# Kernel tuning notes

Hardware: AMD Instinct MI355X
Metric: run time of the kernel (lower is better)

The kernel has to match this reference:

```python
import jax, jax.numpy as jnp
import numpy as np

B = 8192          # batch rows
F0 = 2048         # base input features
E = 512           # embed rows added per recursion level
L = 3             # chain depth
OUT = 2048        # MAIN output dim
NNZ_E = 8192      # nnz per embed sparse weight (~16/row)
NNZ_M = 16384     # nnz of MAIN sparse weight (~8/row)


def _spmm_t(rows, cols, vals, x, n_rows):
    """Compute (W_sparse @ x.T).T = x @ W.T for COO W of shape [n_rows, x.shape[1]].
    out[b, r] = sum_{k: rows[k]==r} vals[k] * x[b, cols[k]]
    """
    contrib = x[:, cols] * vals                     # [B, nnz]
    return jax.ops.segment_sum(contrib.T, rows, num_segments=n_rows).T  # [B, n_rows]


def setup_inputs() -> dict:
    key = jax.random.key(0)
    ks = jax.random.split(key, 12)
    widths = [F0, F0 + E, F0 + 2 * E]               # input width at each recursion level
    inp = {"x": jax.random.normal(ks[0], (B, F0), dtype=jnp.float32)}
    for i, w in enumerate(widths):
        inp[f"emb_rows{i}"] = jax.random.randint(ks[1 + 3 * i], (NNZ_E,), 0, E, dtype=jnp.int32)
        inp[f"emb_cols{i}"] = jax.random.randint(ks[2 + 3 * i], (NNZ_E,), 0, w, dtype=jnp.int32)
        inp[f"emb_vals{i}"] = jax.random.normal(ks[3 + 3 * i], (NNZ_E,), dtype=jnp.float32)
    inp["main_rows"] = jax.random.randint(ks[10], (NNZ_M,), 0, OUT, dtype=jnp.int32)
    inp["main_cols"] = jax.random.randint(ks[11], (NNZ_M,), 0, F0 + 3 * E, dtype=jnp.int32)
    inp["main_vals"] = jax.random.normal(jax.random.fold_in(key, 99), (NNZ_M,), dtype=jnp.float32)
    return inp


def reference(x, emb_rows0, emb_cols0, emb_vals0,
              emb_rows1, emb_cols1, emb_vals1,
              emb_rows2, emb_cols2, emb_vals2,
              main_rows, main_cols, main_vals):
    # Recursive chain unrolled oldest-first: each level sparse-mms its embed
    # weight against the running input and concatenates the result.
    h = x
    for rows, cols, vals in ((emb_rows0, emb_cols0, emb_vals0),
                             (emb_rows1, emb_cols1, emb_vals1),
                             (emb_rows2, emb_cols2, emb_vals2)):
        e = _spmm_t(rows, cols, vals, h, E)         # [B, E]
        h = jnp.concatenate([h, e], axis=1)
    # is_last: pass concatenated features through the MAIN sparse linear
    return _spmm_t(main_rows, main_cols, main_vals, h, OUT)  # [B, OUT]
```

## Files before the change

kernel.cpp:

```cpp
#include <hip/hip_runtime.h>
#include <stdint.h>

#define F0    2048
#define EROWS 512
#define NOUT  2048
#define MROWS 8192

typedef __attribute__((ext_vector_type(8))) short bf16x8;
typedef __attribute__((ext_vector_type(4))) float f32x4;
typedef __attribute__((ext_vector_type(8))) unsigned short u16x8;

typedef const __attribute__((address_space(1))) unsigned char ga_t;
typedef __attribute__((address_space(3))) unsigned char lds_t;

__device__ __forceinline__ void async_load16(const void* g, void* l) {
  __builtin_amdgcn_global_load_lds((ga_t*)g, (lds_t*)l, 16, 0, 0);
}

__device__ __forceinline__ unsigned short f2bf(float f) {
  unsigned int u = __builtin_bit_cast(unsigned int, f);
  u += 0x7fffu + ((u >> 16) & 1u);
  return (unsigned short)(u >> 16);
}

__global__ __launch_bounds__(256) void csr_cast_kernel(
    const int* __restrict__ r0, const int* __restrict__ c0, const float* __restrict__ v0, int n0,
    const int* __restrict__ r1, const int* __restrict__ c1, const float* __restrict__ v1, int n1,
    const int* __restrict__ r2, const int* __restrict__ c2, const float* __restrict__ v2, int n2,
    const int* __restrict__ rm, const int* __restrict__ cm, const float* __restrict__ vm, int nm,
    int* __restrict__ rp_all, int* __restrict__ cc_all, float* __restrict__ cv_all,
    const float* __restrict__ x, unsigned short* __restrict__ Ab)
{
  const int b = blockIdx.x;
  const int tid = threadIdx.x;

  if (b >= 4) {
    const int cb = b - 4;
    const float4* xp = (const float4*)x;
    u16x8* ap = (u16x8*)Ab;
#pragma unroll
    for (int it = 0; it < 4; ++it) {
      int i = cb * 1024 + it * 256 + tid;
      float4 a = xp[2 * i], c = xp[2 * i + 1];
      u16x8 o;
      o[0] = f2bf(a.x); o[1] = f2bf(a.y); o[2] = f2bf(a.z); o[3] = f2bf(a.w);
      o[4] = f2bf(c.x); o[5] = f2bf(c.y); o[6] = f2bf(c.z); o[7] = f2bf(c.w);
      ap[i] = o;
    }
    return;
  }

  const int* rows; const int* cols; const float* vals; int nnz, nrows;
  if      (b == 0) { rows = r0; cols = c0; vals = v0; nnz = n0; nrows = EROWS; }
  else if (b == 1) { rows = r1; cols = c1; vals = v1; nnz = n1; nrows = EROWS; }
  else if (b == 2) { rows = r2; cols = c2; vals = v2; nnz = n2; nrows = EROWS; }
  else             { rows = rm; cols = cm; vals = vm; nnz = nm; nrows = NOUT; }
  int* rp  = rp_all + b * 4096;
  int* cc  = cc_all + b * 8192;
  float* cv = cv_all + b * 8192;

  __shared__ int hist[NOUT + 1];
  __shared__ int tsum[256];

  for (int i = tid; i < nrows; i += 256) hist[i] = 0;
  __syncthreads();

  int k0 = 0;
  for (; k0 + 2048 <= nnz; k0 += 2048) {
    const int kk = k0 + tid * 8;
    int4 ra = *(const int4*)(rows + kk);
    int4 rb = *(const int4*)(rows + kk + 4);
    atomicAdd(&hist[ra.x], 1); atomicAdd(&hist[ra.y], 1);
    atomicAdd(&hist[ra.z], 1); atomicAdd(&hist[ra.w], 1);
    atomicAdd(&hist[rb.x], 1); atomicAdd(&hist[rb.y], 1);
    atomicAdd(&hist[rb.z], 1); atomicAdd(&hist[rb.w], 1);
  }
  for (int k = k0 + tid; k < nnz; k += 256) atomicAdd(&hist[rows[k]], 1);
  __syncthreads();

  const int per = nrows >> 8;
  const int base = tid * per;
  int sum = 0;
  for (int i = 0; i < per; ++i) sum += hist[base + i];
  tsum[tid] = sum;
  __syncthreads();
  for (int off = 1; off < 256; off <<= 1) {
    int add = (tid >= off) ? tsum[tid - off] : 0;
    __syncthreads();
    tsum[tid] += add;
    __syncthreads();
  }
  int run = (tid == 0) ? 0 : tsum[tid - 1];
  for (int i = 0; i < per; ++i) { int h = hist[base + i]; hist[base + i] = run; run += h; }
  __syncthreads();

  for (int i = tid; i < nrows; i += 256) rp[i] = hist[i];
  if (tid == 0) rp[nrows] = nnz;
  __syncthreads();

  k0 = 0;
  for (; k0 + 2048 <= nnz; k0 += 2048) {
    const int kk = k0 + tid * 8;
    int4   ra = *(const int4*)(rows + kk);
    int4   rb = *(const int4*)(rows + kk + 4);
    int4   ca = *(const int4*)(cols + kk);
    int4   cb2 = *(const int4*)(cols + kk + 4);
    float4 va = *(const float4*)(vals + kk);
    float4 vb = *(const float4*)(vals + kk + 4);
    int p;
    p = atomicAdd(&hist[ra.x], 1); cc[p] = ca.x;  cv[p] = va.x;
    p = atomicAdd(&hist[ra.y], 1); cc[p] = ca.y;  cv[p] = va.y;
    p = atomicAdd(&hist[ra.z], 1); cc[p] = ca.z;  cv[p] = va.z;
    p = atomicAdd(&hist[ra.w], 1); cc[p] = ca.w;  cv[p] = va.w;
    p = atomicAdd(&hist[rb.x], 1); cc[p] = cb2.x; cv[p] = vb.x;
    p = atomicAdd(&hist[rb.y], 1); cc[p] = cb2.y; cv[p] = vb.y;
    p = atomicAdd(&hist[rb.z], 1); cc[p] = cb2.z; cv[p] = vb.z;
    p = atomicAdd(&hist[rb.w], 1); cc[p] = cb2.w; cv[p] = vb.w;
  }
  for (int k = k0 + tid; k < nnz; k += 256) {
    int p = atomicAdd(&hist[rows[k]], 1);
    cc[p] = cols[k]; cv[p] = vals[k];
  }
}

template <bool BF16OUT>
__global__ __launch_bounds__(256) void expand_csr_kernel(
    const int* __restrict__ rp, const int* __restrict__ cc,
    const float* __restrict__ cv, const float* __restrict__ Dsrc,
    void* __restrict__ out)
{
  const int r = blockIdx.x;
  const int tid = threadIdx.x;
  __shared__ float acc[F0];
  __shared__ int   icol[128];
  __shared__ float ival[128];
  __shared__ int   icnt;

  float4* a4 = (float4*)acc;
  a4[tid * 2]     = (float4){0.f, 0.f, 0.f, 0.f};
  a4[tid * 2 + 1] = (float4){0.f, 0.f, 0.f, 0.f};
  if (tid == 0) icnt = 0;
  __syncthreads();

  const int s = rp[r], e = rp[r + 1];
  for (int i = s + tid; i < e; i += 256) {
    int c = cc[i]; float v = cv[i];
    if (c < F0) atomicAdd(&acc[c], v);
    else { int p = atomicAdd(&icnt, 1); if (p < 128) { icol[p] = c - F0; ival[p] = v; } }
  }
  __syncthreads();
  int n = icnt; if (n > 128) n = 128;

  float4 q0 = a4[tid * 2], q1 = a4[tid * 2 + 1];
  for (int j = 0; j < n; ++j) {
    const float4* src = (const float4*)(Dsrc + (size_t)icol[j] * F0) + tid * 2;
    float v = ival[j];
    float4 s0 = src[0], s1 = src[1];
    q0.x += v * s0.x; q0.y += v * s0.y; q0.z += v * s0.z; q0.w += v * s0.w;
    q1.x += v * s1.x; q1.y += v * s1.y; q1.z += v * s1.z; q1.w += v * s1.w;
  }

  if (BF16OUT) {
    u16x8 o;
    o[0] = f2bf(q0.x); o[1] = f2bf(q0.y); o[2] = f2bf(q0.z); o[3] = f2bf(q0.w);
    o[4] = f2bf(q1.x); o[5] = f2bf(q1.y); o[6] = f2bf(q1.z); o[7] = f2bf(q1.w);
    ((u16x8*)out)[(size_t)r * 256 + tid] = o;
  } else {
    float4* dst = (float4*)out + (size_t)r * 512 + tid * 2;
    dst[0] = q0; dst[1] = q1;
  }
}

__global__ __launch_bounds__(512, 2) void gemm256_kernel(
    const unsigned short* __restrict__ A, const unsigned short* __restrict__ B,
    float* __restrict__ C)
{
  constexpr int K  = F0;
  constexpr int N  = NOUT;
  constexpr int NT = K / 64;

  extern __shared__ __align__(16) unsigned short lds[];
  unsigned short* sA = lds;
  unsigned short* sB = lds + 32768;

  const int tid  = threadIdx.x;
  const int lane = tid & 63;
  const int w    = tid >> 6;
  const int wr   = w >> 2;
  const int wc   = w & 3;
  const int mm   = lane & 15;
  const int g    = lane >> 4;
  const int sx   = mm & 7;
  const int bm   = blockIdx.y;
  const int bn   = blockIdx.x;

  const unsigned short* Ag = A + (size_t)bm * 256 * K;
  const unsigned short* Bg = B + (size_t)bn * 256 * K;

  const int    r0    = tid >> 3;
  const int    c0    = (tid & 7) ^ (r0 & 7);
  const size_t goff0 = (size_t)r0 * K + c0 * 8;
  const size_t goff1 = goff0 + (size_t)64 * K;
  const int    loff0 = tid * 8;
  const int    loff1 = 4096 + tid * 8;

#define STG(Gb, Sb, buf, h, t) do {                                           \
    async_load16((Gb) + goff0 + (size_t)(h) * 128 * K + (t) * 64,             \
                 (Sb) + (buf) * 16384 + (h) * 8192 + loff0);                  \
    async_load16((Gb) + goff1 + (size_t)(h) * 128 * K + (t) * 64,             \
                 (Sb) + (buf) * 16384 + (h) * 8192 + loff1);                  \
  } while (0)

  const unsigned short* paB = sA + (wr * 128 + mm) * 64;
  const unsigned short* pbB = sB + (wc * 64  + mm) * 64;
  const int s0 = ((0 * 4 + g) ^ sx) * 8;
  const int s1 = ((1 * 4 + g) ^ sx) * 8;

  bf16x8 af[4][2];
  bf16x8 bf0[2][2];
  bf16x8 bf1[2][2];

#define LDA(buf, qm) do {                                                     \
    const unsigned short* p_ = paB + (buf) * 16384 + (qm) * 4096;             \
    _Pragma("unroll") for (int tm = 0; tm < 4; ++tm) {                        \
      af[tm][0] = *(const bf16x8*)(p_ + tm * 1024 + s0);                      \
      af[tm][1] = *(const bf16x8*)(p_ + tm * 1024 + s1);                      \
    } } while (0)

#define LDB(dst, buf, qn) do {                                                \
    const unsigned short* p_ = pbB + (buf) * 16384 + (qn) * 2048;             \
    _Pragma("unroll") for (int tn = 0; tn < 2; ++tn) {                        \
      dst[tn][0] = *(const bf16x8*)(p_ + tn * 1024 + s0);                     \
      dst[tn][1] = *(const bf16x8*)(p_ + tn * 1024 + s1);                     \
    } } while (0)

#define PH_MFMA(qm, qn, bfX) do {                                             \
    __builtin_amdgcn_s_setprio(1);                                            \
    _Pragma("unroll") for (int tm = 0; tm < 4; ++tm)                          \
    _Pragma("unroll") for (int tn = 0; tn < 2; ++tn) {                        \
      acc[(qm)*4+tm][(qn)*2+tn] = __builtin_amdgcn_mfma_f32_16x16x32_bf16(    \
          af[tm][0], bfX[tn][0], acc[(qm)*4+tm][(qn)*2+tn], 0, 0, 0);         \
      acc[(qm)*4+tm][(qn)*2+tn] = __builtin_amdgcn_mfma_f32_16x16x32_bf16(    \
          af[tm][1], bfX[tn][1], acc[(qm)*4+tm][(qn)*2+tn], 0, 0, 0);         \
    }                                                                         \
    __builtin_amdgcn_s_setprio(0);                                            \
  } while (0)

#define BAR        __builtin_amdgcn_s_barrier()
#define LGKM0      asm volatile("s_waitcnt lgkmcnt(0)" ::: "memory")
#define WAIT_VM(n) asm volatile("s_waitcnt vmcnt(" #n ")" ::: "memory")

  f32x4 acc[8][4];
#pragma unroll
  for (int i = 0; i < 8; ++i)
#pragma unroll
    for (int j = 0; j < 4; ++j) acc[i][j] = (f32x4)0.f;

  STG(Ag, sA, 0, 0, 0); STG(Ag, sA, 0, 1, 0);
  STG(Bg, sB, 0, 0, 0); STG(Bg, sB, 0, 1, 0);
  STG(Bg, sB, 1, 0, 1); STG(Bg, sB, 1, 1, 1);
  STG(Ag, sA, 1, 0, 1);
  WAIT_VM(6);
  BAR;

#pragma unroll 2
  for (int t = 0; t < NT; ++t) {
    const int buf  = t & 1;
    const int nbuf = buf ^ 1;

    LDA(buf, 0); LDB(bf0, buf, 0);
    if (t + 1 < NT) STG(Ag, sA, nbuf, 1, t + 1);
    BAR; LGKM0;
    PH_MFMA(0, 0, bf0);
    BAR;

    LDB(bf1, buf, 1);
    BAR; LGKM0;
    PH_MFMA(0, 1, bf1);
    BAR;

    LDA(buf, 1);
    if (t + 2 < NT) STG(Bg, sB, buf, 0, t + 2);
    BAR; LGKM0;
    PH_MFMA(1, 1, bf1);
    BAR;

    if (t + 2 < NT) { STG(Bg, sB, buf, 1, t + 2);
                      STG(Ag, sA, buf, 0, t + 2); }
    BAR;
    PH_MFMA(1, 0, bf0);
    if      (t + 2 < NT) { WAIT_VM(6); }
    else if (t + 1 < NT) { WAIT_VM(0); }
    BAR;
  }

  const int rowb = bm * 256 + wr * 128 + g * 4;
  const int colb = bn * 256 + wc * 64 + mm;
#pragma unroll
  for (int im = 0; im < 8; ++im) {
#pragma unroll
    for (int in2 = 0; in2 < 4; ++in2) {
      const int row = rowb + im * 16;
      const int col = colb + in2 * 16;
#pragma unroll
      for (int r = 0; r < 4; ++r)
        C[(size_t)(row + r) * N + col] = acc[im][in2][r];
    }
  }

#undef STG
#undef LDA
#undef LDB
#undef PH_MFMA
#undef BAR
#undef LGKM0
#undef WAIT_VM
}

extern "C" void kernel_launch(void* const* d_in, const int* in_sizes, int n_in,
                              void* d_out, int out_size, void* d_ws, size_t ws_size,
                              hipStream_t stream)
{
  const float* x   = (const float*)d_in[0];
  const int*   er0 = (const int*)d_in[1];
  const int*   ec0 = (const int*)d_in[2];
  const float* ev0 = (const float*)d_in[3];
  const int*   er1 = (const int*)d_in[4];
  const int*   ec1 = (const int*)d_in[5];
  const float* ev1 = (const float*)d_in[6];
  const int*   er2 = (const int*)d_in[7];
  const int*   ec2 = (const int*)d_in[8];
  const float* ev2 = (const float*)d_in[9];
  const int*   mr  = (const int*)d_in[10];
  const int*   mc  = (const int*)d_in[11];
  const float* mv  = (const float*)d_in[12];
  const int nnz_e0 = in_sizes[1];
  const int nnz_e1 = in_sizes[4];
  const int nnz_e2 = in_sizes[7];
  const int nnz_m  = in_sizes[10];

  int*   rp_all = (int*)d_ws;
  int*   cc_all = rp_all + 4 * 4096;
  float* cv_all = (float*)(cc_all + 48 * 1024);
  float* D      = (float*)(cv_all + 48 * 1024);
  unsigned short* Mb = (unsigned short*)(D + (size_t)3 * EROWS * F0);
  unsigned short* Ab = Mb + (size_t)NOUT * F0;

  hipLaunchKernelGGL(csr_cast_kernel, dim3(4 + 2048), dim3(256), 0, stream,
                     er0, ec0, ev0, nnz_e0,
                     er1, ec1, ev1, nnz_e1,
                     er2, ec2, ev2, nnz_e2,
                     mr,  mc,  mv,  nnz_m,
                     rp_all, cc_all, cv_all, x, Ab);

  hipLaunchKernelGGL((expand_csr_kernel<false>), dim3(EROWS), dim3(256), 0, stream,
                     rp_all + 0 * 4096, cc_all + 0 * 8192, cv_all + 0 * 8192,
                     D, (void*)D);
  hipLaunchKernelGGL((expand_csr_kernel<false>), dim3(EROWS), dim3(256), 0, stream,
                     rp_all + 1 * 4096, cc_all + 1 * 8192, cv_all + 1 * 8192,
                     D, (void*)(D + (size_t)EROWS * F0));
  hipLaunchKernelGGL((expand_csr_kernel<false>), dim3(EROWS), dim3(256), 0, stream,
                     rp_all + 2 * 4096, cc_all + 2 * 8192, cv_all + 2 * 8192,
                     D, (void*)(D + (size_t)2 * EROWS * F0));
  hipLaunchKernelGGL((expand_csr_kernel<true>), dim3(NOUT), dim3(256), 0, stream,
                     rp_all + 3 * 4096, cc_all + 3 * 8192, cv_all + 3 * 8192,
                     D, (void*)Mb);

  hipFuncSetAttribute(reinterpret_cast<const void*>(gemm256_kernel),
                      hipFuncAttributeMaxDynamicSharedMemorySize, 131072);
  hipLaunchKernelGGL(gemm256_kernel, dim3(NOUT / 256, MROWS / 256), dim3(512),
                     131072, stream, Ab, Mb, (float*)d_out);
}
```

Measured before the change: 240.3 us.

## Spread x cast across expand kernels and software-pipeline GEMM LDS fragment loads

```diff
diff --git a/kernel.cpp b/kernel.cpp
--- a/kernel.cpp
+++ b/kernel.cpp
@@ -28,27 +28,10 @@
     const int* __restrict__ r1, const int* __restrict__ c1, const float* __restrict__ v1, int n1,
     const int* __restrict__ r2, const int* __restrict__ c2, const float* __restrict__ v2, int n2,
     const int* __restrict__ rm, const int* __restrict__ cm, const float* __restrict__ vm, int nm,
-    int* __restrict__ rp_all, int* __restrict__ cc_all, float* __restrict__ cv_all,
-    const float* __restrict__ x, unsigned short* __restrict__ Ab)
+    int* __restrict__ rp_all, int* __restrict__ cc_all, float* __restrict__ cv_all)
 {
   const int b = blockIdx.x;
   const int tid = threadIdx.x;
-
-  if (b >= 4) {
-    const int cb = b - 4;
-    const float4* xp = (const float4*)x;
-    u16x8* ap = (u16x8*)Ab;
-#pragma unroll
-    for (int it = 0; it < 4; ++it) {
-      int i = cb * 1024 + it * 256 + tid;
-      float4 a = xp[2 * i], c = xp[2 * i + 1];
-      u16x8 o;
-      o[0] = f2bf(a.x); o[1] = f2bf(a.y); o[2] = f2bf(a.z); o[3] = f2bf(a.w);
-      o[4] = f2bf(c.x); o[5] = f2bf(c.y); o[6] = f2bf(c.z); o[7] = f2bf(c.w);
-      ap[i] = o;
-    }
-    return;
-  }
 
   const int* rows; const int* cols; const float* vals; int nnz, nrows;
   if      (b == 0) { rows = r0; cols = c0; vals = v0; nnz = n0; nrows = EROWS; }
@@ -127,10 +110,29 @@
 __global__ __launch_bounds__(256) void expand_csr_kernel(
     const int* __restrict__ rp, const int* __restrict__ cc,
     const float* __restrict__ cv, const float* __restrict__ Dsrc,
-    void* __restrict__ out)
+    void* __restrict__ out, int nrows,
+    const float* __restrict__ x, unsigned short* __restrict__ Ab, int cast_base)
 {
-  const int r = blockIdx.x;
+  const int b = blockIdx.x;
   const int tid = threadIdx.x;
+
+  if (b >= nrows) {
+    const int cb = cast_base + (b - nrows);
+    const float4* xp = (const float4*)x;
+    u16x8* ap = (u16x8*)Ab;
+#pragma unroll
+    for (int it = 0; it < 4; ++it) {
+      int i = cb * 1024 + it * 256 + tid;
+      float4 a = xp[2 * i], c = xp[2 * i + 1];
+      u16x8 o;
+      o[0] = f2bf(a.x); o[1] = f2bf(a.y); o[2] = f2bf(a.z); o[3] = f2bf(a.w);
+      o[4] = f2bf(c.x); o[5] = f2bf(c.y); o[6] = f2bf(c.z); o[7] = f2bf(c.w);
+      ap[i] = o;
+    }
+    return;
+  }
+
+  const int r = b;
   __shared__ float acc[F0];
   __shared__ int   icol[128];
   __shared__ float ival[128];
@@ -216,15 +218,16 @@
   const int s0 = ((0 * 4 + g) ^ sx) * 8;
   const int s1 = ((1 * 4 + g) ^ sx) * 8;
 
-  bf16x8 af[4][2];
+  bf16x8 afP[4][2];
+  bf16x8 afQ[4][2];
   bf16x8 bf0[2][2];
   bf16x8 bf1[2][2];
 
-#define LDA(buf, qm) do {                                                     \
+#define LDA(dst, buf, qm) do {                                                \
     const unsigned short* p_ = paB + (buf) * 16384 + (qm) * 4096;             \
     _Pragma("unroll") for (int tm = 0; tm < 4; ++tm) {                        \
-      af[tm][0] = *(const bf16x8*)(p_ + tm * 1024 + s0);                      \
-      af[tm][1] = *(const bf16x8*)(p_ + tm * 1024 + s1);                      \
+      dst[tm][0] = *(const bf16x8*)(p_ + tm * 1024 + s0);                     \
+      dst[tm][1] = *(const bf16x8*)(p_ + tm * 1024 + s1);                     \
     } } while (0)
 
 #define LDB(dst, buf, qn) do {                                                \
@@ -234,20 +237,21 @@
       dst[tn][1] = *(const bf16x8*)(p_ + tn * 1024 + s1);                     \
     } } while (0)
 
-#define PH_MFMA(qm, qn, bfX) do {                                             \
+#define MFMA_Q(qm, qn, afX, bfX) do {                                         \
     __builtin_amdgcn_s_setprio(1);                                            \
     _Pragma("unroll") for (int tm = 0; tm < 4; ++tm)                          \
     _Pragma("unroll") for (int tn = 0; tn < 2; ++tn) {                        \
       acc[(qm)*4+tm][(qn)*2+tn] = __builtin_amdgcn_mfma_f32_16x16x32_bf16(    \
-          af[tm][0], bfX[tn][0], acc[(qm)*4+tm][(qn)*2+tn], 0, 0, 0);         \
+          afX[tm][0], bfX[tn][0], acc[(qm)*4+tm][(qn)*2+tn], 0, 0, 0);        \
       acc[(qm)*4+tm][(qn)*2+tn] = __builtin_amdgcn_mfma_f32_16x16x32_bf16(    \
-          af[tm][1], bfX[tn][1], acc[(qm)*4+tm][(qn)*2+tn], 0, 0, 0);         \
+          afX[tm][1], bfX[tn][1], acc[(qm)*4+tm][(qn)*2+tn], 0, 0, 0);        \
     }                                                                         \
     __builtin_amdgcn_s_setprio(0);                                            \
   } while (0)
 
-#define BAR        __builtin_amdgcn_s_barrier()
-#define LGKM0      asm volatile("s_waitcnt lgkmcnt(0)" ::: "memory")
+#define CFENCE     asm volatile("" ::: "memory")
+#define BAR        do { CFENCE; __builtin_amdgcn_s_barrier(); CFENCE; } while (0)
+#define SCHED0     __builtin_amdgcn_sched_barrier(0)
 #define WAIT_VM(n) asm volatile("s_waitcnt vmcnt(" #n ")" ::: "memory")
 
   f32x4 acc[8][4];
@@ -256,42 +260,53 @@
 #pragma unroll
     for (int j = 0; j < 4; ++j) acc[i][j] = (f32x4)0.f;
 
-  STG(Ag, sA, 0, 0, 0); STG(Ag, sA, 0, 1, 0);
-  STG(Bg, sB, 0, 0, 0); STG(Bg, sB, 0, 1, 0);
-  STG(Bg, sB, 1, 0, 1); STG(Bg, sB, 1, 1, 1);
+  STG(Bg, sB, 0, 0, 0);
+  STG(Bg, sB, 0, 1, 0);
+  STG(Ag, sA, 0, 0, 0);
+  STG(Ag, sA, 0, 1, 0);
+  STG(Bg, sB, 1, 0, 1);
+  STG(Bg, sB, 1, 1, 1);
   STG(Ag, sA, 1, 0, 1);
   WAIT_VM(6);
   BAR;
+  SCHED0;
+  LDA(afP, 0, 0);
+  LDB(bf0, 0, 0);
 
 #pragma unroll 2
   for (int t = 0; t < NT; ++t) {
     const int buf  = t & 1;
     const int nbuf = buf ^ 1;
 
-    LDA(buf, 0); LDB(bf0, buf, 0);
     if (t + 1 < NT) STG(Ag, sA, nbuf, 1, t + 1);
-    BAR; LGKM0;
-    PH_MFMA(0, 0, bf0);
+    if (t + 1 < NT) { WAIT_VM(8); } else { WAIT_VM(0); }
+    SCHED0;
+    LDB(bf1, buf, 1);
+    MFMA_Q(0, 0, afP, bf0);
+
+    BAR; SCHED0;
+    LDA(afQ, buf, 1);
+    MFMA_Q(0, 1, afP, bf1);
+
     BAR;
-
-    LDB(bf1, buf, 1);
-    BAR; LGKM0;
-    PH_MFMA(0, 1, bf1);
+    if (t + 2 < NT) STG(Bg, sB, buf, 0, t + 2);
+    MFMA_Q(1, 0, afQ, bf0);
+
     BAR;
-
-    LDA(buf, 1);
-    if (t + 2 < NT) STG(Bg, sB, buf, 0, t + 2);
-    BAR; LGKM0;
-    PH_MFMA(1, 1, bf1);
-    BAR;
-
-    if (t + 2 < NT) { STG(Bg, sB, buf, 1, t + 2);
-                      STG(Ag, sA, buf, 0, t + 2); }
-    BAR;
-    PH_MFMA(1, 0, bf0);
-    if      (t + 2 < NT) { WAIT_VM(6); }
-    else if (t + 1 < NT) { WAIT_VM(0); }
-    BAR;
+    if (t + 2 < NT) {
+      STG(Bg, sB, buf, 1, t + 2);
+      STG(Ag, sA, buf, 0, t + 2);
+      WAIT_VM(6);
+      BAR; SCHED0;
+      LDA(afP, nbuf, 0);
+      LDB(bf0, nbuf, 0);
+    } else if (t + 1 < NT) {
+      WAIT_VM(0);
+      BAR; SCHED0;
+      LDA(afP, nbuf, 0);
+      LDB(bf0, nbuf, 0);
+    }
+    MFMA_Q(1, 1, afQ, bf1);
   }
 
   const int rowb = bm * 256 + wr * 128 + g * 4;
@@ -311,9 +326,10 @@
 #undef STG
 #undef LDA
 #undef LDB
-#undef PH_MFMA
+#undef MFMA_Q
+#undef CFENCE
 #undef BAR
-#undef LGKM0
+#undef SCHED0
 #undef WAIT_VM
 }
 
@@ -346,25 +362,25 @@
   unsigned short* Mb = (unsigned short*)(D + (size_t)3 * EROWS * F0);
   unsigned short* Ab = Mb + (size_t)NOUT * F0;
 
-  hipLaunchKernelGGL(csr_cast_kernel, dim3(4 + 2048), dim3(256), 0, stream,
+  hipLaunchKernelGGL(csr_cast_kernel, dim3(4), dim3(256), 0, stream,
                      er0, ec0, ev0, nnz_e0,
                      er1, ec1, ev1, nnz_e1,
                      er2, ec2, ev2, nnz_e2,
                      mr,  mc,  mv,  nnz_m,
-                     rp_all, cc_all, cv_all, x, Ab);
-
-  hipLaunchKernelGGL((expand_csr_kernel<false>), dim3(EROWS), dim3(256), 0, stream,
+                     rp_all, cc_all, cv_all);
+
+  hipLaunchKernelGGL((expand_csr_kernel<false>), dim3(EROWS + 512), dim3(256), 0, stream,
                      rp_all + 0 * 4096, cc_all + 0 * 8192, cv_all + 0 * 8192,
-                     D, (void*)D);
-  hipLaunchKernelGGL((expand_csr_kernel<false>), dim3(EROWS), dim3(256), 0, stream,
+                     D, (void*)D, EROWS, x, Ab, 0);
+  hipLaunchKernelGGL((expand_csr_kernel<false>), dim3(EROWS + 512), dim3(256), 0, stream,
                      rp_all + 1 * 4096, cc_all + 1 * 8192, cv_all + 1 * 8192,
-                     D, (void*)(D + (size_t)EROWS * F0));
-  hipLaunchKernelGGL((expand_csr_kernel<false>), dim3(EROWS), dim3(256), 0, stream,
+                     D, (void*)(D + (size_t)EROWS * F0), EROWS, x, Ab, 512);
+  hipLaunchKernelGGL((expand_csr_kernel<false>), dim3(EROWS + 512), dim3(256), 0, stream,
                      rp_all + 2 * 4096, cc_all + 2 * 8192, cv_all + 2 * 8192,
-                     D, (void*)(D + (size_t)2 * EROWS * F0));
-  hipLaunchKernelGGL((expand_csr_kernel<true>), dim3(NOUT), dim3(256), 0, stream,
+                     D, (void*)(D + (size_t)2 * EROWS * F0), EROWS, x, Ab, 1024);
+  hipLaunchKernelGGL((expand_csr_kernel<true>), dim3(NOUT + 512), dim3(256), 0, stream,
                      rp_all + 3 * 4096, cc_all + 3 * 8192, cv_all + 3 * 8192,
-                     D, (void*)Mb);
+                     D, (void*)Mb, NOUT, x, Ab, 1536);
 
   hipFuncSetAttribute(reinterpret_cast<const void*>(gemm256_kernel),
                       hipFuncAttributeMaxDynamicSharedMemorySize, 131072);
```

Result: no change. 237.3 us (-1.2%).
